# Optimization experiments

Hardware: AMD Instinct MI355X
Metric: run time of the kernel (lower is better)

## Reference

```python
import jax, jax.numpy as jnp
import numpy as np

B, S, DIM = 1, 2048, 2048
H, KVH = 32, 8
D = DIM // H  # 64


def setup_inputs() -> dict:
    key = jax.random.key(0)
    ks = jax.random.split(key, 10)
    x = jax.random.normal(ks[0], (B, S, DIM), dtype=jnp.float32)
    # RoPE frequencies: theta=10000, per LLaMA
    inv_freq = 1.0 / (10000.0 ** (np.arange(0, D, 2, dtype=np.float32) / D))  # (D/2,)
    angles = np.arange(S, dtype=np.float32)[:, None] * inv_freq[None, :]      # (S, D/2)
    freqs_cos = jnp.asarray(np.cos(angles))
    freqs_sin = jnp.asarray(np.sin(angles))
    # causal mask (1,1,S,S), 1 = keep, 0 = masked
    mask = jnp.tril(jnp.ones((S, S), dtype=jnp.int32))[None, None, :, :]
    w = 0.02
    Wq = jax.random.normal(ks[1], (DIM, H * D), dtype=jnp.float32) * w
    bq = jnp.zeros((H * D,), dtype=jnp.float32)
    Wk = jax.random.normal(ks[2], (DIM, KVH * D), dtype=jnp.float32) * w
    bk = jnp.zeros((KVH * D,), dtype=jnp.float32)
    Wv = jax.random.normal(ks[3], (DIM, KVH * D), dtype=jnp.float32) * w
    bv = jnp.zeros((KVH * D,), dtype=jnp.float32)
    Wo = jax.random.normal(ks[4], (H * D, DIM), dtype=jnp.float32) * w
    bo = jnp.zeros((DIM,), dtype=jnp.float32)
    return {"x": x, "freqs_cos": freqs_cos, "freqs_sin": freqs_sin, "mask": mask,
            "Wq": Wq, "bq": bq, "Wk": Wk, "bk": bk, "Wv": Wv, "bv": bv, "Wo": Wo, "bo": bo}


def _rope(t, cos, sin):
    # t: (B, S, h, D) with D even; rotate consecutive pairs (real form of complex mult)
    tr = t.reshape(*t.shape[:-1], -1, 2)          # (B,S,h,D/2,2)
    c = cos[None, :, None, :]                     # (1,S,1,D/2)
    s = sin[None, :, None, :]
    o0 = tr[..., 0] * c - tr[..., 1] * s
    o1 = tr[..., 0] * s + tr[..., 1] * c
    return jnp.stack([o0, o1], axis=-1).reshape(t.shape)


def reference(x, freqs_cos, freqs_sin, mask, Wq, bq, Wk, bk, Wv, bv, Wo, bo):
    b, s, dim = x.shape
    scale = 1.0 / jnp.sqrt(jnp.asarray(D, dtype=x.dtype))
    q = (x @ Wq + bq).reshape(b, s, H, D)
    k = (x @ Wk + bk).reshape(b, s, KVH, D)
    v = (x @ Wv + bv).reshape(b, s, KVH, D)
    q = _rope(q, freqs_cos, freqs_sin)
    k = _rope(k, freqs_cos, freqs_sin)
    # GQA: repeat kv heads to match query heads
    rep = H // KVH
    k = jnp.repeat(k, rep, axis=2)
    v = jnp.repeat(v, rep, axis=2)
    # to (B, H, S, D)
    q = q.transpose(0, 2, 1, 3)
    k = k.transpose(0, 2, 1, 3)
    v = v.transpose(0, 2, 1, 3)
    scores = jnp.einsum('bhqd,bhkd->bhqk', q, k) * scale   # (B,H,S,S)
    neg = jnp.asarray(jnp.finfo(scores.dtype).min, dtype=scores.dtype)
    scores = jnp.where(mask == 0, neg, scores)
    attn = jax.nn.softmax(scores, axis=-1)
    out = jnp.einsum('bhqk,bhkd->bhqd', attn, v)            # (B,H,S,D)
    out = out.transpose(0, 2, 1, 3).reshape(b, s, H * D)
    return out @ Wo + bo
```

## Files before the change

### kernel.cpp

```cpp
#include <hip/hip_runtime.h>
#include <stdint.h>

#define S_LEN 2048
#define DIM   2048
#define NHEAD 32
#define KVHEAD 8
#define HDIM  64
#define NQKV  3072

typedef __attribute__((ext_vector_type(8))) __bf16 bf16x8;
typedef __attribute__((ext_vector_type(4))) float f32x4;
typedef __attribute__((ext_vector_type(8))) unsigned short u16x8;

#if __has_builtin(__builtin_amdgcn_exp2f)
#define EXP2F(x) __builtin_amdgcn_exp2f(x)
#else
#define EXP2F(x) exp2f(x)
#endif

__device__ __forceinline__ unsigned short f2bf(float f) {
  unsigned u = __builtin_bit_cast(unsigned, f);
  unsigned r = (u + 0x7FFFu + ((u >> 16) & 1u)) >> 16;
  return (unsigned short)r;
}
__device__ __forceinline__ float bf2f(unsigned short h) {
  unsigned u = ((unsigned)h) << 16;
  return __builtin_bit_cast(float, u);
}

__device__ __forceinline__ void gl_lds16(const void* g, void* l) {
  __builtin_amdgcn_global_load_lds(
      (const __attribute__((address_space(1))) unsigned*)g,
      (__attribute__((address_space(3))) unsigned*)l, 16, 0, 0);
}


__global__ void convert_x_kernel(const float* __restrict__ x,
                                 unsigned short* __restrict__ xb, int n4) {
  int i = blockIdx.x * blockDim.x + threadIdx.x;
  if (i >= n4) return;
  float4 v = ((const float4*)x)[i];
  ushort4 o;
  o.x = f2bf(v.x); o.y = f2bf(v.y); o.z = f2bf(v.z); o.w = f2bf(v.w);
  ((ushort4*)xb)[i] = o;
}

__global__ void bias_concat_kernel(const float* __restrict__ bq,
                                   const float* __restrict__ bk,
                                   const float* __restrict__ bv,
                                   float* __restrict__ bqkv) {
  int i = blockIdx.x * blockDim.x + threadIdx.x;
  if (i >= NQKV) return;
  bqkv[i] = (i < 2048) ? bq[i] : (i < 2560 ? bk[i - 2048] : bv[i - 2560]);
}

__global__ void transpose_weights_kernel(const float* __restrict__ Wq,
                                         const float* __restrict__ Wk,
                                         const float* __restrict__ Wv,
                                         const float* __restrict__ Wo,
                                         unsigned short* __restrict__ WqkvT,
                                         unsigned short* __restrict__ WoT) {
  __shared__ float t[32][33];
  int bx = blockIdx.x, by = blockIdx.y;
  const float* src; int C, sc, dbase; unsigned short* dst;
  if (bx < 64)      { src = Wq; C = 2048; sc = bx * 32;        dst = WqkvT; dbase = sc; }
  else if (bx < 80) { src = Wk; C = 512;  sc = (bx - 64) * 32; dst = WqkvT; dbase = 2048 + sc; }
  else if (bx < 96) { src = Wv; C = 512;  sc = (bx - 80) * 32; dst = WqkvT; dbase = 2560 + sc; }
  else              { src = Wo; C = 2048; sc = (bx - 96) * 32; dst = WoT;   dbase = sc; }
  int tx = threadIdx.x, ty = threadIdx.y;
#pragma unroll
  for (int j = 0; j < 32; j += 8)
    t[ty + j][tx] = src[(size_t)(by * 32 + ty + j) * C + sc + tx];
  __syncthreads();
#pragma unroll
  for (int j = 0; j < 32; j += 8)
    dst[(size_t)(dbase + ty + j) * 2048 + by * 32 + tx] = f2bf(t[tx][ty + j]);
}

__global__ void transpose_b2b_kernel(const unsigned short* __restrict__ src, int lds_,
                                     int R, int C,
                                     unsigned short* __restrict__ dst, int ldd) {
  __shared__ unsigned short t[32][33];
  int bx = blockIdx.x * 32;
  int by = blockIdx.y * 32;
  int tx = threadIdx.x, ty = threadIdx.y;
#pragma unroll
  for (int j = 0; j < 32; j += 8)
    t[ty + j][tx] = src[(size_t)(by + ty + j) * lds_ + bx + tx];
  __syncthreads();
#pragma unroll
  for (int j = 0; j < 32; j += 8)
    dst[(size_t)(bx + ty + j) * ldd + by + tx] = t[tx][ty + j];
}

__global__ void rope_kernel(unsigned short* __restrict__ qkv,
                            const float* __restrict__ fc,
                            const float* __restrict__ fs) {
  int idx = blockIdx.x * blockDim.x + threadIdx.x;
  int row = idx / 1280;
  int p   = idx - row * 1280;
  if (row >= S_LEN) return;
  int col = (p < 1024) ? (p * 2) : (2048 + (p - 1024) * 2);
  int fi = p & 31;
  float c  = fc[row * 32 + fi];
  float sn = fs[row * 32 + fi];
  unsigned* base = (unsigned*)(qkv + (size_t)row * NQKV + col);
  unsigned v = *base;
  float x0 = bf2f((unsigned short)(v & 0xFFFF));
  float x1 = bf2f((unsigned short)(v >> 16));
  unsigned short o0 = f2bf(x0 * c - x1 * sn);
  unsigned short o1 = f2bf(x0 * sn + x1 * c);
  *base = (unsigned)o0 | ((unsigned)o1 << 16);
}

template <int OUT_BF16>
__global__ __launch_bounds__(512) void gemm_bt_kernel(
    const unsigned short* __restrict__ A,
    const unsigned short* __restrict__ BT,
    const float* __restrict__ bias,
    void* __restrict__ Cc, int M, int N, int K) {
  __shared__ char smem[65536];
  const int tid = threadIdx.x;
  const int lane = tid & 63;
  const int wid = tid >> 6;
  const int kh = wid >> 2;
  const int wsub = wid & 3;
  const int wm = wsub >> 1, wn = wsub & 1;
  const int rowA0 = blockIdx.x * 128;
  const int rowB0 = blockIdx.y * 128;
  const int l15 = lane & 15, l4 = lane >> 4;
  const int kcol = kh * 64 + l4 * 16;

  f32x4 acc[4][4];
#pragma unroll
  for (int i = 0; i < 4; i++)
#pragma unroll
    for (int j = 0; j < 4; j++) acc[i][j] = (f32x4){0.f, 0.f, 0.f, 0.f};

  const int nK = K >> 6;

  auto stage = [&](int buf, int kt) {
    const char* Ab = (const char*)A + ((size_t)rowA0 * K + (size_t)kt * 64) * 2;
    const char* Bb = (const char*)BT + ((size_t)rowB0 * K + (size_t)kt * 64) * 2;
#pragma unroll
    for (int h = 0; h < 2; ++h) {
      int o = h * 8192 + tid * 16;
      int r = o >> 7;
      int cb = (o & 127) ^ ((r & 7) << 4);
      gl_lds16(Ab + (size_t)r * (K * 2) + cb, smem + buf * 16384 + o);
      gl_lds16(Bb + (size_t)r * (K * 2) + cb, smem + 32768 + buf * 16384 + o);
    }
  };

  stage(0, 0);
  __syncthreads();
  int buf = 0;

  for (int kt = 0; kt < nK; ++kt) {
    if (kt + 1 < nK) stage(buf ^ 1, kt + 1);

    bf16x8 af[4], bfr[4];
#pragma unroll
    for (int i = 0; i < 4; i++) {
      int ra = wm * 64 + i * 16 + l15;
      int rb = wn * 64 + i * 16 + l15;
      af[i]  = *(const bf16x8*)(smem + buf * 16384 + ra * 128 + (kcol ^ ((ra & 7) << 4)));
      bfr[i] = *(const bf16x8*)(smem + 32768 + buf * 16384 + rb * 128 + (kcol ^ ((rb & 7) << 4)));
    }
#pragma unroll
    for (int i = 0; i < 4; i++)
#pragma unroll
      for (int j = 0; j < 4; j++)
        acc[i][j] = __builtin_amdgcn_mfma_f32_16x16x32_bf16(af[i], bfr[j], acc[i][j], 0, 0, 0);
    __syncthreads();
    buf ^= 1;
  }

  f32x4* eps = (f32x4*)smem;
  if (kh == 1) {
#pragma unroll
    for (int i = 0; i < 4; i++)
#pragma unroll
      for (int j = 0; j < 4; j++)
        eps[wsub * 1024 + (i * 4 + j) * 64 + lane] = acc[i][j];
  }
  __syncthreads();
  if (kh == 0) {
#pragma unroll
    for (int i = 0; i < 4; i++) {
      int row0 = rowA0 + wm * 64 + i * 16 + l4 * 4;
#pragma unroll
      for (int j = 0; j < 4; j++) {
        f32x4 oth = eps[wsub * 1024 + (i * 4 + j) * 64 + lane];
        int col = rowB0 + wn * 64 + j * 16 + l15;
        float bv_ = bias[col];
#pragma unroll
        for (int r = 0; r < 4; r++) {
          float v = acc[i][j][r] + oth[r] + bv_;
          size_t idx = (size_t)(row0 + r) * N + col;
          if (OUT_BF16) ((unsigned short*)Cc)[idx] = f2bf(v);
          else          ((float*)Cc)[idx] = v;
        }
      }
    }
  }
}

__global__ __launch_bounds__(512) void attn_kernel(
    const unsigned short* __restrict__ qkv,
    const unsigned short* __restrict__ VT,
    unsigned short* __restrict__ O) {
  __shared__ unsigned short Ks[3][64 * 64];
  __shared__ unsigned short VTs[3][64 * 64];
  __shared__ unsigned short Ps[8][16 * 64];

  const int tid = threadIdx.x;
  const int lane = tid & 63;
  const int w = tid >> 6;
  const int l15 = lane & 15, l4 = lane >> 4;
  const int kvh = blockIdx.x >> 5;
  const int pr  = blockIdx.x & 31;
  const int h = kvh * 4 + (w >> 1);
  const int qsub = (w & 1) * 16;

  auto issue = [&](int buf, int t) {
    int kvb = t * 64;
    int o = tid << 4;
    int r = o >> 7;
    int cb = (o & 127) ^ ((r & 7) << 4);
    gl_lds16((const char*)qkv + ((size_t)(kvb + r) * NQKV + 2048 + kvh * 64) * 2 + cb,
             (char*)&Ks[buf][0] + o);
    gl_lds16((const char*)VT + ((size_t)(kvh * 64 + r) * S_LEN + kvb) * 2 + cb,
             (char*)&VTs[buf][0] + o);
  };

#pragma unroll 1
  for (int ph = 0; ph < 2; ++ph) {
    const int qt = ph ? pr : 63 - pr;
    const int nt = (qt >> 1) + 1;
    const int qbase = qt * 32;

    bf16x8 qf[2];
    {
      const unsigned short* qrow = qkv + (size_t)(qbase + qsub + l15) * NQKV + h * 64;
#pragma unroll
      for (int kf = 0; kf < 2; ++kf) {
        u16x8 raw = *(const u16x8*)(qrow + kf * 32 + l4 * 8);
        u16x8 sc;
#pragma unroll
        for (int i = 0; i < 8; i++) sc[i] = f2bf(bf2f(raw[i]) * 0.1803368801111f);
        qf[kf] = __builtin_bit_cast(bf16x8, sc);
      }
    }

    f32x4 oacc[4];
    float lsum[4];
#pragma unroll
    for (int d = 0; d < 4; d++) oacc[d] = (f32x4){0.f, 0.f, 0.f, 0.f};
#pragma unroll
    for (int r = 0; r < 4; r++) lsum[r] = 0.f;

    __syncthreads();
    issue(0, 0);
    if (nt > 1) issue(1, 1);

    for (int t = 0; t < nt; ++t) {
      if (t + 1 < nt) { asm volatile("s_waitcnt vmcnt(2)" ::: "memory"); }
      else            { asm volatile("s_waitcnt vmcnt(0)" ::: "memory"); }
      __builtin_amdgcn_s_barrier();
      asm volatile("" ::: "memory");
      if (t + 2 < nt) issue((t + 2) % 3, t + 2);
      const int buf = t % 3;

      f32x4 sacc[4];
#pragma unroll
      for (int nf = 0; nf < 4; nf++) sacc[nf] = (f32x4){0.f, 0.f, 0.f, 0.f};
#pragma unroll
      for (int nf = 0; nf < 4; nf++) {
#pragma unroll
        for (int kf = 0; kf < 2; kf++) {
          int row = nf * 16 + l15;
          bf16x8 kb = *(const bf16x8*)((const char*)&Ks[buf][0] + row * 128 +
                                       ((kf * 64 + l4 * 16) ^ ((row & 7) << 4)));
          sacc[nf] = __builtin_amdgcn_mfma_f32_16x16x32_bf16(qf[kf], kb, sacc[nf], 0, 0, 0);
        }
      }

      if (t == nt - 1) {
        int kvb = t * 64;
#pragma unroll
        for (int nf = 0; nf < 4; nf++) {
          int kvpos = kvb + nf * 16 + l15;
#pragma unroll
          for (int r = 0; r < 4; r++) {
            int qpos = qbase + qsub + l4 * 4 + r;
            if (kvpos > qpos) sacc[nf][r] = -3.0e38f;
          }
        }
      }

#pragma unroll
      for (int nf = 0; nf < 4; nf++) {
#pragma unroll
        for (int r = 0; r < 4; r++) {
          float p = EXP2F(sacc[nf][r]);
          lsum[r] += p;
          int rr = l4 * 4 + r;
          int b = ((nf * 16 + l15) * 2) ^ ((rr & 7) << 4);
          *(unsigned short*)((char*)&Ps[w][0] + rr * 128 + b) = f2bf(p);
        }
      }

#pragma unroll
      for (int kf = 0; kf < 2; kf++) {
        bf16x8 pf = *(const bf16x8*)((const char*)&Ps[w][0] + l15 * 128 +
                                     ((kf * 64 + l4 * 16) ^ ((l15 & 7) << 4)));
#pragma unroll
        for (int df = 0; df < 4; df++) {
          int row = df * 16 + l15;
          bf16x8 vb = *(const bf16x8*)((const char*)&VTs[buf][0] + row * 128 +
                                       ((kf * 64 + l4 * 16) ^ ((row & 7) << 4)));
          oacc[df] = __builtin_amdgcn_mfma_f32_16x16x32_bf16(pf, vb, oacc[df], 0, 0, 0);
        }
      }
    }

#pragma unroll
    for (int r = 0; r < 4; r++) {
#pragma unroll
      for (int off = 1; off < 16; off <<= 1) lsum[r] += __shfl_xor(lsum[r], off, 64);
    }

#pragma unroll
    for (int r = 0; r < 4; r++) {
      float inv = 1.0f / lsum[r];
      int qpos = qbase + qsub + l4 * 4 + r;
#pragma unroll
      for (int df = 0; df < 4; df++)
        O[(size_t)qpos * DIM + h * 64 + df * 16 + l15] = f2bf(oacc[df][r] * inv);
    }
  }
}

extern "C" void kernel_launch(void* const* d_in, const int* in_sizes, int n_in,
                              void* d_out, int out_size, void* d_ws, size_t ws_size,
                              hipStream_t stream) {
  const float* x  = (const float*)d_in[0];
  const float* fc = (const float*)d_in[1];
  const float* fs = (const float*)d_in[2];
  const float* Wq = (const float*)d_in[4];
  const float* bq = (const float*)d_in[5];
  const float* Wk = (const float*)d_in[6];
  const float* bk = (const float*)d_in[7];
  const float* Wv = (const float*)d_in[8];
  const float* bv = (const float*)d_in[9];
  const float* Wo = (const float*)d_in[10];
  const float* bo = (const float*)d_in[11];
  float* out = (float*)d_out;

  char* ws = (char*)d_ws;
  unsigned short* xb    = (unsigned short*)(ws + 0);
  unsigned short* WqkvT = (unsigned short*)(ws + 8388608);
  unsigned short* WoT   = (unsigned short*)(ws + 20971520);
  float*          bqkv  = (float*)(ws + 29360128);
  unsigned short* qkv   = (unsigned short*)(ws + 29372416);
  unsigned short* VT    = WqkvT;
  unsigned short* attn  = xb;

  convert_x_kernel<<<4096, 256, 0, stream>>>(x, xb, 2048 * 2048 / 4);
  bias_concat_kernel<<<12, 256, 0, stream>>>(bq, bk, bv, bqkv);
  dim3 tb(32, 8);
  transpose_weights_kernel<<<dim3(160, 64), tb, 0, stream>>>(Wq, Wk, Wv, Wo, WqkvT, WoT);

  gemm_bt_kernel<1><<<dim3(16, 24), 512, 0, stream>>>(xb, WqkvT, bqkv, qkv, 2048, 3072, 2048);
  rope_kernel<<<(2048 * 1280) / 256, 256, 0, stream>>>(qkv, fc, fs);
  transpose_b2b_kernel<<<dim3(16, 64), tb, 0, stream>>>(qkv + 2560, NQKV, 2048, 512, VT, 2048);
  attn_kernel<<<256, 512, 0, stream>>>(qkv, VT, attn);
  gemm_bt_kernel<0><<<dim3(16, 16), 512, 0, stream>>>(attn, WoT, bo, out, 2048, 2048, 2048);
}
```

Baseline: 238.5 us.

## Fuse prep and rope/VT kernels; keep attention P in registers via permlane

Merges the x conversion, bias concat and weight transpose into one prep launch, and merges RoPE with the V transpose into a single launch, cutting launch count from seven to four. In attention, QK^T is computed transposed (K as A operand) so the probabilities can be packed with v_cvt_pk_bf16_f32 and rearranged with permlane swaps directly into the A-operand layout for the PV MFMA. This removes the per-tile LDS round trip for P and the per-row 16-lane sum reductions. It relies on gfx950-specific permlane instructions and a correct lane mapping.

```diff
diff --git a/kernel.cpp b/kernel.cpp
--- a/kernel.cpp
+++ b/kernel.cpp
@@ -11,6 +11,7 @@
 typedef __attribute__((ext_vector_type(8))) __bf16 bf16x8;
 typedef __attribute__((ext_vector_type(4))) float f32x4;
 typedef __attribute__((ext_vector_type(8))) unsigned short u16x8;
+typedef __attribute__((ext_vector_type(4))) unsigned int u32x4;
 
 #if __has_builtin(__builtin_amdgcn_exp2f)
 #define EXP2F(x) __builtin_amdgcn_exp2f(x)
@@ -34,83 +35,85 @@
       (__attribute__((address_space(3))) unsigned*)l, 16, 0, 0);
 }
 
-
-__global__ void convert_x_kernel(const float* __restrict__ x,
-                                 unsigned short* __restrict__ xb, int n4) {
-  int i = blockIdx.x * blockDim.x + threadIdx.x;
-  if (i >= n4) return;
-  float4 v = ((const float4*)x)[i];
-  ushort4 o;
-  o.x = f2bf(v.x); o.y = f2bf(v.y); o.z = f2bf(v.z); o.w = f2bf(v.w);
-  ((ushort4*)xb)[i] = o;
-}
-
-__global__ void bias_concat_kernel(const float* __restrict__ bq,
-                                   const float* __restrict__ bk,
-                                   const float* __restrict__ bv,
-                                   float* __restrict__ bqkv) {
-  int i = blockIdx.x * blockDim.x + threadIdx.x;
-  if (i >= NQKV) return;
-  bqkv[i] = (i < 2048) ? bq[i] : (i < 2560 ? bk[i - 2048] : bv[i - 2560]);
-}
-
-__global__ void transpose_weights_kernel(const float* __restrict__ Wq,
-                                         const float* __restrict__ Wk,
-                                         const float* __restrict__ Wv,
-                                         const float* __restrict__ Wo,
-                                         unsigned short* __restrict__ WqkvT,
-                                         unsigned short* __restrict__ WoT) {
-  __shared__ float t[32][33];
-  int bx = blockIdx.x, by = blockIdx.y;
-  const float* src; int C, sc, dbase; unsigned short* dst;
-  if (bx < 64)      { src = Wq; C = 2048; sc = bx * 32;        dst = WqkvT; dbase = sc; }
-  else if (bx < 80) { src = Wk; C = 512;  sc = (bx - 64) * 32; dst = WqkvT; dbase = 2048 + sc; }
-  else if (bx < 96) { src = Wv; C = 512;  sc = (bx - 80) * 32; dst = WqkvT; dbase = 2560 + sc; }
-  else              { src = Wo; C = 2048; sc = (bx - 96) * 32; dst = WoT;   dbase = sc; }
-  int tx = threadIdx.x, ty = threadIdx.y;
-#pragma unroll
-  for (int j = 0; j < 32; j += 8)
-    t[ty + j][tx] = src[(size_t)(by * 32 + ty + j) * C + sc + tx];
-  __syncthreads();
-#pragma unroll
-  for (int j = 0; j < 32; j += 8)
-    dst[(size_t)(dbase + ty + j) * 2048 + by * 32 + tx] = f2bf(t[tx][ty + j]);
-}
-
-__global__ void transpose_b2b_kernel(const unsigned short* __restrict__ src, int lds_,
-                                     int R, int C,
-                                     unsigned short* __restrict__ dst, int ldd) {
-  __shared__ unsigned short t[32][33];
-  int bx = blockIdx.x * 32;
-  int by = blockIdx.y * 32;
-  int tx = threadIdx.x, ty = threadIdx.y;
-#pragma unroll
-  for (int j = 0; j < 32; j += 8)
-    t[ty + j][tx] = src[(size_t)(by + ty + j) * lds_ + bx + tx];
-  __syncthreads();
-#pragma unroll
-  for (int j = 0; j < 32; j += 8)
-    dst[(size_t)(bx + ty + j) * ldd + by + tx] = t[tx][ty + j];
-}
-
-__global__ void rope_kernel(unsigned short* __restrict__ qkv,
-                            const float* __restrict__ fc,
-                            const float* __restrict__ fs) {
-  int idx = blockIdx.x * blockDim.x + threadIdx.x;
-  int row = idx / 1280;
-  int p   = idx - row * 1280;
-  if (row >= S_LEN) return;
-  int col = (p < 1024) ? (p * 2) : (2048 + (p - 1024) * 2);
-  int fi = p & 31;
-  float c  = fc[row * 32 + fi];
-  float sn = fs[row * 32 + fi];
-  unsigned* base = (unsigned*)(qkv + (size_t)row * NQKV + col);
-  unsigned v = *base;
-  float x0 = bf2f((unsigned short)(v & 0xFFFF));
-  float x1 = bf2f((unsigned short)(v >> 16));
-  unsigned short o0 = f2bf(x0 * c - x1 * sn);
-  unsigned short o1 = f2bf(x0 * sn + x1 * c);
-  *base = (unsigned)o0 | ((unsigned)o1 << 16);
+__global__ void prep_kernel(const float* __restrict__ x,
+                            const float* __restrict__ bq,
+                            const float* __restrict__ bk,
+                            const float* __restrict__ bv,
+                            const float* __restrict__ Wq,
+                            const float* __restrict__ Wk,
+                            const float* __restrict__ Wv,
+                            const float* __restrict__ Wo,
+                            unsigned short* __restrict__ xb,
+                            unsigned short* __restrict__ WqkvT,
+                            unsigned short* __restrict__ WoT,
+                            float* __restrict__ bqkv) {
+  int idx = blockIdx.x;
+  int tid = threadIdx.x;
+  if (idx < 10240) {
+    __shared__ float t[32][33];
+    int bx = idx >> 6, by = idx & 63;
+    const float* src; int C, sc, dbase; unsigned short* dst;
+    if (bx < 64)      { src = Wq; C = 2048; sc = bx * 32;        dst = WqkvT; dbase = sc; }
+    else if (bx < 80) { src = Wk; C = 512;  sc = (bx - 64) * 32; dst = WqkvT; dbase = 2048 + sc; }
+    else if (bx < 96) { src = Wv; C = 512;  sc = (bx - 80) * 32; dst = WqkvT; dbase = 2560 + sc; }
+    else              { src = Wo; C = 2048; sc = (bx - 96) * 32; dst = WoT;   dbase = sc; }
+    int tx = tid & 31, ty = tid >> 5;
+#pragma unroll
+    for (int j = 0; j < 32; j += 8)
+      t[ty + j][tx] = src[(size_t)(by * 32 + ty + j) * C + sc + tx];
+    __syncthreads();
+#pragma unroll
+    for (int j = 0; j < 32; j += 8)
+      dst[(size_t)(dbase + ty + j) * 2048 + by * 32 + tx] = f2bf(t[tx][ty + j]);
+  } else if (idx < 14336) {
+    int i = (idx - 10240) * 256 + tid;
+    float4 v = ((const float4*)x)[i];
+    ushort4 o;
+    o.x = f2bf(v.x); o.y = f2bf(v.y); o.z = f2bf(v.z); o.w = f2bf(v.w);
+    ((ushort4*)xb)[i] = o;
+  } else {
+    int i = (idx - 14336) * 256 + tid;
+    if (i < NQKV)
+      bqkv[i] = (i < 2048) ? bq[i] : (i < 2560 ? bk[i - 2048] : bv[i - 2560]);
+  }
+}
+
+__global__ void rope_vt_kernel(unsigned short* __restrict__ qkv,
+                               const float* __restrict__ fc,
+                               const float* __restrict__ fs,
+                               unsigned short* __restrict__ VT) {
+  int idx = blockIdx.x;
+  int tid = threadIdx.x;
+  if (idx < 10240) {
+    int i = idx * 256 + tid;
+    int row = i / 1280;
+    int p   = i - row * 1280;
+    int col = (p < 1024) ? (p * 2) : (2048 + (p - 1024) * 2);
+    int fi = p & 31;
+    float c  = fc[row * 32 + fi];
+    float sn = fs[row * 32 + fi];
+    unsigned* base = (unsigned*)(qkv + (size_t)row * NQKV + col);
+    unsigned v = *base;
+    float x0 = bf2f((unsigned short)(v & 0xFFFF));
+    float x1 = bf2f((unsigned short)(v >> 16));
+    unsigned short o0 = f2bf(x0 * c - x1 * sn);
+    unsigned short o1 = f2bf(x0 * sn + x1 * c);
+    *base = (unsigned)o0 | ((unsigned)o1 << 16);
+  } else {
+    __shared__ unsigned short t[32][33];
+    int sub = idx - 10240;
+    int bx = (sub & 15) * 32;
+    int by = (sub >> 4) * 32;
+    int tx = tid & 31, ty = tid >> 5;
+    const unsigned short* src = qkv + 2560;
+#pragma unroll
+    for (int j = 0; j < 32; j += 8)
+      t[ty + j][tx] = src[(size_t)(by + ty + j) * 3072 + bx + tx];
+    __syncthreads();
+#pragma unroll
+    for (int j = 0; j < 32; j += 8)
+      VT[(size_t)(bx + ty + j) * 2048 + by + tx] = t[tx][ty + j];
+  }
 }
 
 template <int OUT_BF16>
@@ -212,7 +215,6 @@
     unsigned short* __restrict__ O) {
   __shared__ unsigned short Ks[3][64 * 64];
   __shared__ unsigned short VTs[3][64 * 64];
-  __shared__ unsigned short Ps[8][16 * 64];
 
   const int tid = threadIdx.x;
   const int lane = tid & 63;
@@ -254,11 +256,9 @@
     }
 
     f32x4 oacc[4];
-    float lsum[4];
+    float lsum = 0.f;
 #pragma unroll
     for (int d = 0; d < 4; d++) oacc[d] = (f32x4){0.f, 0.f, 0.f, 0.f};
-#pragma unroll
-    for (int r = 0; r < 4; r++) lsum[r] = 0.f;
 
     __syncthreads();
     issue(0, 0);
@@ -282,18 +282,18 @@
           int row = nf * 16 + l15;
           bf16x8 kb = *(const bf16x8*)((const char*)&Ks[buf][0] + row * 128 +
                                        ((kf * 64 + l4 * 16) ^ ((row & 7) << 4)));
-          sacc[nf] = __builtin_amdgcn_mfma_f32_16x16x32_bf16(qf[kf], kb, sacc[nf], 0, 0, 0);
+          sacc[nf] = __builtin_amdgcn_mfma_f32_16x16x32_bf16(kb, qf[kf], sacc[nf], 0, 0, 0);
         }
       }
 
       if (t == nt - 1) {
         int kvb = t * 64;
+        int qpos = qbase + qsub + l15;
 #pragma unroll
         for (int nf = 0; nf < 4; nf++) {
-          int kvpos = kvb + nf * 16 + l15;
 #pragma unroll
           for (int r = 0; r < 4; r++) {
-            int qpos = qbase + qsub + l4 * 4 + r;
+            int kvpos = kvb + nf * 16 + l4 * 4 + r;
             if (kvpos > qpos) sacc[nf][r] = -3.0e38f;
           }
         }
@@ -304,36 +304,50 @@
 #pragma unroll
         for (int r = 0; r < 4; r++) {
           float p = EXP2F(sacc[nf][r]);
-          lsum[r] += p;
-          int rr = l4 * 4 + r;
-          int b = ((nf * 16 + l15) * 2) ^ ((rr & 7) << 4);
-          *(unsigned short*)((char*)&Ps[w][0] + rr * 128 + b) = f2bf(p);
-        }
-      }
-
-#pragma unroll
-      for (int kf = 0; kf < 2; kf++) {
-        bf16x8 pf = *(const bf16x8*)((const char*)&Ps[w][0] + l15 * 128 +
-                                     ((kf * 64 + l4 * 16) ^ ((l15 & 7) << 4)));
+          lsum += p;
+          sacc[nf][r] = p;
+        }
+      }
+
+      unsigned wds[4][2];
+#pragma unroll
+      for (int nf = 0; nf < 4; nf++)
+#pragma unroll
+        for (int m = 0; m < 2; m++)
+          asm("v_cvt_pk_bf16_f32 %0, %1, %2"
+              : "=v"(wds[nf][m]) : "v"(sacc[nf][2 * m]), "v"(sacc[nf][2 * m + 1]));
+
+      bf16x8 paf[2];
+#pragma unroll
+      for (int kc = 0; kc < 2; kc++) {
+        unsigned a0 = wds[2 * kc][0], b0 = wds[2 * kc + 1][0];
+        unsigned a1 = wds[2 * kc][1], b1 = wds[2 * kc + 1][1];
+        asm("v_permlane32_swap_b32 %0, %1" : "+v"(a0), "+v"(b0));
+        asm("v_permlane16_swap_b32 %0, %1" : "+v"(a0), "+v"(b0));
+        asm("v_permlane32_swap_b32 %0, %1" : "+v"(a1), "+v"(b1));
+        asm("v_permlane16_swap_b32 %0, %1" : "+v"(a1), "+v"(b1));
+        u32x4 afu = (u32x4){a0, a1, b0, b1};
+        paf[kc] = __builtin_bit_cast(bf16x8, afu);
+      }
+
+#pragma unroll
+      for (int kc = 0; kc < 2; kc++) {
 #pragma unroll
         for (int df = 0; df < 4; df++) {
           int row = df * 16 + l15;
           bf16x8 vb = *(const bf16x8*)((const char*)&VTs[buf][0] + row * 128 +
-                                       ((kf * 64 + l4 * 16) ^ ((row & 7) << 4)));
-          oacc[df] = __builtin_amdgcn_mfma_f32_16x16x32_bf16(pf, vb, oacc[df], 0, 0, 0);
-        }
-      }
-    }
+                                       ((kc * 64 + l4 * 16) ^ ((row & 7) << 4)));
+          oacc[df] = __builtin_amdgcn_mfma_f32_16x16x32_bf16(paf[kc], vb, oacc[df], 0, 0, 0);
+        }
+      }
+    }
+
+    lsum += __shfl_xor(lsum, 16, 64);
+    lsum += __shfl_xor(lsum, 32, 64);
 
 #pragma unroll
     for (int r = 0; r < 4; r++) {
-#pragma unroll
-      for (int off = 1; off < 16; off <<= 1) lsum[r] += __shfl_xor(lsum[r], off, 64);
-    }
-
-#pragma unroll
-    for (int r = 0; r < 4; r++) {
-      float inv = 1.0f / lsum[r];
+      float inv = 1.0f / __shfl(lsum, l4 * 4 + r, 16);
       int qpos = qbase + qsub + l4 * 4 + r;
 #pragma unroll
       for (int df = 0; df < 4; df++)
@@ -367,14 +381,10 @@
   unsigned short* VT    = WqkvT;
   unsigned short* attn  = xb;
 
-  convert_x_kernel<<<4096, 256, 0, stream>>>(x, xb, 2048 * 2048 / 4);
-  bias_concat_kernel<<<12, 256, 0, stream>>>(bq, bk, bv, bqkv);
-  dim3 tb(32, 8);
-  transpose_weights_kernel<<<dim3(160, 64), tb, 0, stream>>>(Wq, Wk, Wv, Wo, WqkvT, WoT);
-
+  prep_kernel<<<14348, 256, 0, stream>>>(x, bq, bk, bv, Wq, Wk, Wv, Wo,
+                                         xb, WqkvT, WoT, bqkv);
   gemm_bt_kernel<1><<<dim3(16, 24), 512, 0, stream>>>(xb, WqkvT, bqkv, qkv, 2048, 3072, 2048);
-  rope_kernel<<<(2048 * 1280) / 256, 256, 0, stream>>>(qkv, fc, fs);
-  transpose_b2b_kernel<<<dim3(16, 64), tb, 0, stream>>>(qkv + 2560, NQKV, 2048, 512, VT, 2048);
+  rope_vt_kernel<<<11264, 256, 0, stream>>>(qkv, fc, fs, VT);
   attn_kernel<<<256, 512, 0, stream>>>(qkv, VT, attn);
   gemm_bt_kernel<0><<<dim3(16, 16), 512, 0, stream>>>(attn, WoT, bo, out, 2048, 2048, 2048);
 }
```

New measurement: 228.0 us. 4.4% less time.
